# Optimization experiments

Hardware: AMD Instinct MI355X
Metric: run time of the kernel (lower is better)

## Reference

```python
import jax, jax.numpy as jnp
import numpy as np

PERIOD = 15          # hardcoded in the torch module's forward: STL(series, 15)
N_SEASONAL = 7       # statsmodels STL default seasonal smoother length
N_TREND = 29         # smallest odd >= 1.5*p/(1-1.5/7) = 28.64 -> 29 (statsmodels default)
N_LOWPASS = 17       # smallest odd > period (statsmodels default)
N_INNER = 2          # statsmodels: robust=False -> 2 inner iterations, 0 outer


def _loess_matrix(n, q, ts):
    """Dense linear operator for degree-1 LOESS smoothing of a length-n series
    evaluated at (possibly out-of-range) integer positions ts. Non-robust LOESS is
    linear in y, so smoothing == matmul with this constant matrix."""
    M = np.zeros((len(ts), n), dtype=np.float64)
    qq = min(q, n)
    for i, t in enumerate(ts):
        left = int(np.clip(t - (q - 1) // 2, 0, n - qq))
        right = left + qq - 1
        h = max(t - left, right - t)
        if q > n:
            h += (q - n) / 2.0
        xs = np.arange(left, right + 1, dtype=np.float64)
        w = np.clip(1.0 - (np.abs(xs - t) / h) ** 3, 0.0, None) ** 3  # tricube
        w = w / w.sum()
        xbar = (w * xs).sum()
        var = (w * (xs - xbar) ** 2).sum()
        a = w.copy()
        if var > 1e-12:  # degree-1 local linear fit; fall back to deg-0 if degenerate
            a = w * (1.0 + (t - xbar) * (xs - xbar) / var)
        M[i, left:right + 1] = a
    return M.astype(np.float32)


def _ma(x, k):
    """Moving average of window k along last axis (valid mode)."""
    cs = jnp.cumsum(x, axis=-1)
    cs = jnp.concatenate([jnp.zeros(x.shape[:-1] + (1,), x.dtype), cs], axis=-1)
    return (cs[..., k:] - cs[..., :-k]) / k


def setup_inputs() -> dict:
    key = jax.random.key(0)
    x = jax.random.normal(key, (128, 480, 256), dtype=jnp.float32)  # [B, T, C]
    return {"x": x}


def reference(x):
    B, T, Cc = x.shape
    p = PERIOD
    n_sub = T // p  # cycle-subseries length; T chosen divisible by period

    # Constant LOESS smoothing operators (numpy, baked in as jit constants)
    M_seas = jnp.asarray(_loess_matrix(n_sub, N_SEASONAL, np.arange(-1, n_sub + 1)))  # (n_sub+2, n_sub)
    M_lp = jnp.asarray(_loess_matrix(T, N_LOWPASS, np.arange(T)))                     # (T, T)
    M_trend = jnp.asarray(_loess_matrix(T, N_TREND, np.arange(T)))                    # (T, T)

    y = jnp.transpose(x, (0, 2, 1))  # [B, C, T]
    trend = jnp.zeros_like(y)
    seasonal = jnp.zeros_like(y)

    for _ in range(N_INNER):  # STL inner loop (Cleveland 1990, non-robust)
        # 1. detrend
        D = y - trend
        # 2. cycle-subseries LOESS smoothing, extended one period each side
        Dsub = D.reshape(B, Cc, n_sub, p)                      # subseries along axis 2
        Cext = jnp.einsum('sn,bcnp->bcsp', M_seas, Dsub)       # [B,C,n_sub+2,p]
        Cext = Cext.reshape(B, Cc, (n_sub + 2) * p)            # time order, length T+2p
        # 3. low-pass: MA(p) x2, MA(3), then LOESS(n_l)
        lp = _ma(_ma(_ma(Cext, p), p), 3)                      # length T
        L = jnp.einsum('tn,bcn->bct', M_lp, lp)
        # 4. seasonal = smoothed subseries (center T) minus low-pass
        seasonal = Cext[..., p:p + T] - L
        # 5+6. deseasonalize and trend LOESS
        trend = jnp.einsum('tn,bcn->bct', M_trend, y - seasonal)

    resid = y - seasonal - trend
    seas_plus_resid = jnp.transpose(seasonal + resid, (0, 2, 1))  # [B, T, C]
    trend_out = jnp.transpose(trend, (0, 2, 1))
    return (seas_plus_resid, trend_out)
```

## Files before the change

### kernel.cpp

```cpp
#include <hip/hip_runtime.h>
#include <hip/hip_bf16.h>
#include <stdint.h>

#define TLEN 480
#define NB 128
#define NC 256

typedef short bf16x8 __attribute__((ext_vector_type(8)));
typedef float f32x4 __attribute__((ext_vector_type(4)));

__device__ inline unsigned short f2bf(float f) {
    union { float f; uint32_t u; } v; v.f = f;
    uint32_t u = v.u;
    return (unsigned short)((u + 0x7fffu + ((u >> 16) & 1u)) >> 16);
}

__device__ void loess_row(int t, int n, int q, float* row) {
    int qq = q < n ? q : n;
    int left = t - (q - 1) / 2;
    if (left < 0) left = 0;
    if (left > n - qq) left = n - qq;
    int right = left + qq - 1;
    int h = (t - left) > (right - t) ? (t - left) : (right - t);
    double w[29];
    double wsum = 0.0;
    for (int i = 0; i < qq; ++i) {
        double dist = fabs((double)(left + i - t)) / (double)h;
        double u = 1.0 - dist * dist * dist;
        if (u < 0.0) u = 0.0;
        double wv = u * u * u;
        w[i] = wv; wsum += wv;
    }
    for (int i = 0; i < qq; ++i) w[i] /= wsum;
    double xbar = 0.0;
    for (int i = 0; i < qq; ++i) xbar += w[i] * (double)(left + i);
    double var = 0.0;
    for (int i = 0; i < qq; ++i) { double d = (double)(left + i) - xbar; var += w[i] * d * d; }
    if (var > 1e-12) {
        double tb = (double)t - xbar;
        for (int i = 0; i < qq; ++i) {
            double d = (double)(left + i) - xbar;
            row[left + i] = (float)(w[i] * (1.0 + tb * d / var));
        }
    } else {
        for (int i = 0; i < qq; ++i) row[left + i] = (float)w[i];
    }
}

__global__ void k_zero(float* p, int n) {
    int id = blockIdx.x * 256 + threadIdx.x;
    if (id < n) p[id] = 0.0f;
}

__global__ void k_loess(float* Ms, float* w3, float* Mlp, float* Mt) {
    int i = threadIdx.x;
    if (i < 34) {
        loess_row(i - 1, 32, 7, Ms + i * 32);
    } else if (i < 34 + 480) {
        int t = i - 34;
        loess_row(t, TLEN, 17, Mlp + (size_t)t * TLEN);
    } else if (i < 34 + 960) {
        int t = i - 514;
        loess_row(t, TLEN, 29, Mt + (size_t)t * TLEN);
    } else if (i == 1000) {
        for (int d = 0; d <= 30; ++d) {
            int cnt = 0;
            for (int c = 0; c < 3; ++c)
                for (int a = 0; a < 15; ++a) {
                    int b = d - a - c;
                    if (b >= 0 && b < 15) cnt++;
                }
            w3[d] = (float)((double)cnt / 675.0);
        }
    }
}

__global__ void k_G(const float* __restrict__ Ms, const float* __restrict__ w3, float* __restrict__ G) {
    int id = blockIdx.x * 256 + threadIdx.x;
    if (id >= TLEN * TLEN) return;
    int i = id / TLEN, u = id - i * TLEN;
    int ju = u % 15, nu = u / 15;
    float acc = 0.0f;
    for (int s = 0; s < 34; ++s) {
        int d = s * 15 + ju - i;
        if (d >= 0 && d <= 30) acc += Ms[s * 32 + nu] * w3[d];
    }
    G[id] = acc;
}

__global__ void k_S(const float* __restrict__ Ms, const float* __restrict__ Mlp,
                    const float* __restrict__ G, float* __restrict__ S) {
    int id = blockIdx.x * 256 + threadIdx.x;
    if (id >= TLEN * TLEN) return;
    int t = id / TLEN, u = id - t * TLEN;
    int lo = t - 8;
    if (lo < 0) lo = 0;
    if (lo > TLEN - 17) lo = TLEN - 17;
    float acc = 0.0f;
    for (int k = 0; k < 17; ++k)
        acc += Mlp[(size_t)t * TLEN + lo + k] * G[(size_t)(lo + k) * TLEN + u];
    float val = -acc;
    if (t % 15 == u % 15) val += Ms[(1 + t / 15) * 32 + (u / 15)];
    S[id] = val;
}

__global__ void k_VU(const float* __restrict__ Mt, const float* __restrict__ S,
                     float* __restrict__ U, float* __restrict__ V) {
    int id = blockIdx.x * 256 + threadIdx.x;
    if (id >= TLEN * TLEN) return;
    int t = id / TLEN, u = id - t * TLEN;
    int lo = t - 14;
    if (lo < 0) lo = 0;
    if (lo > TLEN - 29) lo = TLEN - 29;
    float acc = 0.0f;
    for (int k = 0; k < 29; ++k)
        acc += Mt[(size_t)t * TLEN + lo + k] * S[(size_t)(lo + k) * TLEN + u];
    V[id] = acc;
    U[id] = Mt[id] - acc;
}

__global__ void k_A(const float* __restrict__ U, const float* __restrict__ V,
                    unsigned short* __restrict__ Abf) {
    __shared__ float Vs[16][17];
    __shared__ float Us[16][17];
    int tx = threadIdx.x, ty = threadIdx.y;
    int u = blockIdx.x * 16 + tx;
    int t = blockIdx.y * 16 + ty;
    float acc = 0.0f;
    for (int kt = 0; kt < 30; ++kt) {
        Vs[ty][tx] = V[(size_t)t * TLEN + kt * 16 + tx];
        Us[ty][tx] = U[(size_t)(kt * 16 + ty) * TLEN + u];
        __syncthreads();
        #pragma unroll
        for (int e = 0; e < 16; ++e) acc += Vs[ty][e] * Us[e][tx];
        __syncthreads();
    }
    Abf[(size_t)t * TLEN + u] = f2bf(U[(size_t)t * TLEN + u] + acc);
}

__global__ void k_tr(const float* __restrict__ x, unsigned short* __restrict__ Xt) {
    __shared__ unsigned short Tt[32 * 36];
    int b = blockIdx.z, s0 = blockIdx.y * 32, c0 = blockIdx.x * 32;
    int i = threadIdx.x;
    int r = i >> 3, cg = i & 7;
    float4 v = *(const float4*)(x + (((size_t)b * TLEN + s0 + r) * NC + c0 + cg * 4));
    Tt[(cg * 4 + 0) * 36 + r] = f2bf(v.x);
    Tt[(cg * 4 + 1) * 36 + r] = f2bf(v.y);
    Tt[(cg * 4 + 2) * 36 + r] = f2bf(v.z);
    Tt[(cg * 4 + 3) * 36 + r] = f2bf(v.w);
    __syncthreads();
    int cl = i >> 3, ch = i & 7;
    ushort4 o = *(const ushort4*)&Tt[cl * 36 + ch * 4];
    *(ushort4*)(Xt + (((size_t)b * NC + c0 + cl) * TLEN + s0 + ch * 4)) = o;
}

__global__ __launch_bounds__(256, 2)
void k_gemm(const unsigned short* __restrict__ A, const unsigned short* __restrict__ Xt,
            const float* __restrict__ x, float* __restrict__ out0, float* __restrict__ out1) {
    int b = blockIdx.y;
    int t0 = blockIdx.x * 48;
    int tid = threadIdx.x;
    int wave = tid >> 6, lane = tid & 63;
    int lane15 = lane & 15, quad = lane >> 4;
    int cbase = wave * 64;

    const unsigned short* ap[3];
    #pragma unroll
    for (int i = 0; i < 3; ++i)
        ap[i] = A + (size_t)(t0 + i * 16 + lane15) * TLEN + quad * 8;
    const unsigned short* bp[4];
    #pragma unroll
    for (int j = 0; j < 4; ++j)
        bp[j] = Xt + ((size_t)b * NC + cbase + j * 16 + lane15) * TLEN + quad * 8;

    f32x4 acc[3][4] = {};
    for (int k0 = 0; k0 < TLEN; k0 += 32) {
        bf16x8 af[3], bf[4];
        #pragma unroll
        for (int i = 0; i < 3; ++i) af[i] = *(const bf16x8*)(ap[i] + k0);
        #pragma unroll
        for (int j = 0; j < 4; ++j) bf[j] = *(const bf16x8*)(bp[j] + k0);
        #pragma unroll
        for (int i = 0; i < 3; ++i)
            #pragma unroll
            for (int j = 0; j < 4; ++j)
                acc[i][j] = __builtin_amdgcn_mfma_f32_16x16x32_bf16(af[i], bf[j], acc[i][j], 0, 0, 0);
    }

    #pragma unroll
    for (int i = 0; i < 3; ++i) {
        #pragma unroll
        for (int r = 0; r < 4; ++r) {
            int t = t0 + i * 16 + quad * 4 + r;
            size_t rowbase = ((size_t)b * TLEN + t) * NC;
            #pragma unroll
            for (int j = 0; j < 4; ++j) {
                int c = cbase + j * 16 + lane15;
                float v = acc[i][j][r];
                out1[rowbase + c] = v;
                out0[rowbase + c] = x[rowbase + c] - v;
            }
        }
    }
}

extern "C" void kernel_launch(void* const* d_in, const int* in_sizes, int n_in,
                              void* d_out, int out_size, void* d_ws, size_t ws_size,
                              hipStream_t stream) {
    const float* x = (const float*)d_in[0];
    float* out0 = (float*)d_out;
    float* out1 = (float*)d_out + (size_t)NB * TLEN * NC;

    char* ws = (char*)d_ws;
    size_t oXt = 0;
    size_t oMs = 31457280;
    size_t oW3 = oMs + 4352;
    size_t oLp = oW3 + 128;
    size_t oMt = oLp + 921600;
    size_t oG  = oMt + 921600;
    size_t oS  = oG + 921600;
    size_t oU  = oS + 921600;
    size_t oV  = oU + 921600;
    size_t oA  = oV + 921600;

    unsigned short* Xt = (unsigned short*)(ws + oXt);
    float* Ms  = (float*)(ws + oMs);
    float* w3  = (float*)(ws + oW3);
    float* Mlp = (float*)(ws + oLp);
    float* Mt  = (float*)(ws + oMt);
    float* G   = (float*)(ws + oG);
    float* S   = (float*)(ws + oS);
    float* U   = (float*)(ws + oU);
    float* V   = (float*)(ws + oV);
    unsigned short* Abf = (unsigned short*)(ws + oA);

    int nzero = (4352 + 128 + 921600 * 2) / 4;
    k_zero<<<(nzero + 255) / 256, 256, 0, stream>>>((float*)(ws + oMs), nzero);
    k_loess<<<1, 1024, 0, stream>>>(Ms, w3, Mlp, Mt);
    k_G<<<900, 256, 0, stream>>>(Ms, w3, G);
    k_S<<<900, 256, 0, stream>>>(Ms, Mlp, G, S);
    k_VU<<<900, 256, 0, stream>>>(Mt, S, U, V);
    k_A<<<dim3(30, 30), dim3(16, 16), 0, stream>>>(U, V, Abf);
    k_tr<<<dim3(8, 15, NB), 256, 0, stream>>>(x, Xt);
    k_gemm<<<dim3(10, NB), 256, 0, stream>>>(Abf, Xt, x, out0, out1);
}
```

Baseline: 316.4 us.

## Compact LOESS weights, fuse G into S, swap GEMM operands for vector stores

Stores the LOESS operators as compact banded weights instead of dense 480x480 matrices. This drops the zeroing kernel and the separate G kernel by computing the G entries inline in k_S. The GEMM swaps operand roles so each lane's accumulator holds four consecutive channels, which allows float4 loads of x and float4 stores of both outputs instead of scalar ones. It also changes the grid order to batch-major and raises launch bounds to 4 blocks per unit, which risks register pressure.

New measurement: 289.5 us. -8.5%, faster.

```diff
diff --git a/kernel.cpp b/kernel.cpp
--- a/kernel.cpp
+++ b/kernel.cpp
@@ -8,61 +8,66 @@
 
 typedef short bf16x8 __attribute__((ext_vector_type(8)));
 typedef float f32x4 __attribute__((ext_vector_type(4)));
-
-__device__ inline unsigned short f2bf(float f) {
+typedef unsigned short u16;
+
+__device__ inline u16 f2bf(float f) {
     union { float f; uint32_t u; } v; v.f = f;
     uint32_t u = v.u;
-    return (unsigned short)((u + 0x7fffu + ((u >> 16) & 1u)) >> 16);
-}
-
-__device__ void loess_row(int t, int n, int q, float* row) {
-    int qq = q < n ? q : n;
+    return (u16)((u + 0x7fffu + ((u >> 16) & 1u)) >> 16);
+}
+
+__device__ int loess_w(int t, int n, int q, float* out) {
     int left = t - (q - 1) / 2;
     if (left < 0) left = 0;
-    if (left > n - qq) left = n - qq;
-    int right = left + qq - 1;
+    if (left > n - q) left = n - q;
+    int right = left + q - 1;
     int h = (t - left) > (right - t) ? (t - left) : (right - t);
     double w[29];
     double wsum = 0.0;
-    for (int i = 0; i < qq; ++i) {
+    for (int i = 0; i < q; ++i) {
         double dist = fabs((double)(left + i - t)) / (double)h;
         double u = 1.0 - dist * dist * dist;
         if (u < 0.0) u = 0.0;
         double wv = u * u * u;
         w[i] = wv; wsum += wv;
     }
-    for (int i = 0; i < qq; ++i) w[i] /= wsum;
+    for (int i = 0; i < q; ++i) w[i] /= wsum;
     double xbar = 0.0;
-    for (int i = 0; i < qq; ++i) xbar += w[i] * (double)(left + i);
+    for (int i = 0; i < q; ++i) xbar += w[i] * (double)(left + i);
     double var = 0.0;
-    for (int i = 0; i < qq; ++i) { double d = (double)(left + i) - xbar; var += w[i] * d * d; }
+    for (int i = 0; i < q; ++i) { double d = (double)(left + i) - xbar; var += w[i] * d * d; }
     if (var > 1e-12) {
         double tb = (double)t - xbar;
-        for (int i = 0; i < qq; ++i) {
+        for (int i = 0; i < q; ++i) {
             double d = (double)(left + i) - xbar;
-            row[left + i] = (float)(w[i] * (1.0 + tb * d / var));
+            out[i] = (float)(w[i] * (1.0 + tb * d / var));
         }
     } else {
-        for (int i = 0; i < qq; ++i) row[left + i] = (float)w[i];
-    }
-}
-
-__global__ void k_zero(float* p, int n) {
-    int id = blockIdx.x * 256 + threadIdx.x;
-    if (id < n) p[id] = 0.0f;
-}
-
-__global__ void k_loess(float* Ms, float* w3, float* Mlp, float* Mt) {
-    int i = threadIdx.x;
-    if (i < 34) {
-        loess_row(i - 1, 32, 7, Ms + i * 32);
-    } else if (i < 34 + 480) {
-        int t = i - 34;
-        loess_row(t, TLEN, 17, Mlp + (size_t)t * TLEN);
-    } else if (i < 34 + 960) {
-        int t = i - 514;
-        loess_row(t, TLEN, 29, Mt + (size_t)t * TLEN);
-    } else if (i == 1000) {
+        for (int i = 0; i < q; ++i) out[i] = (float)w[i];
+    }
+    return left;
+}
+
+__global__ void k_loess(float* Ms, float* w3, float* MlpC, float* MtC) {
+    int gid = blockIdx.x * 256 + threadIdx.x;
+    if (gid < 34) {
+        float wl[7];
+        int left = loess_w(gid - 1, 32, 7, wl);
+        float* row = Ms + gid * 32;
+        #pragma unroll
+        for (int i = 0; i < 32; ++i) row[i] = 0.0f;
+        for (int i = 0; i < 7; ++i) row[left + i] = wl[i];
+    } else if (gid < 514) {
+        int t = gid - 34;
+        float wl[17];
+        loess_w(t, TLEN, 17, wl);
+        for (int i = 0; i < 17; ++i) MlpC[t * 17 + i] = wl[i];
+    } else if (gid < 994) {
+        int t = gid - 514;
+        float wl[29];
+        loess_w(t, TLEN, 29, wl);
+        for (int i = 0; i < 29; ++i) MtC[t * 29 + i] = wl[i];
+    } else if (gid == 994) {
         for (int d = 0; d <= 30; ++d) {
             int cnt = 0;
             for (int c = 0; c < 3; ++c)
@@ -75,52 +80,52 @@
     }
 }
 
-__global__ void k_G(const float* __restrict__ Ms, const float* __restrict__ w3, float* __restrict__ G) {
-    int id = blockIdx.x * 256 + threadIdx.x;
-    if (id >= TLEN * TLEN) return;
-    int i = id / TLEN, u = id - i * TLEN;
-    int ju = u % 15, nu = u / 15;
-    float acc = 0.0f;
-    for (int s = 0; s < 34; ++s) {
-        int d = s * 15 + ju - i;
-        if (d >= 0 && d <= 30) acc += Ms[s * 32 + nu] * w3[d];
-    }
-    G[id] = acc;
-}
-
-__global__ void k_S(const float* __restrict__ Ms, const float* __restrict__ Mlp,
-                    const float* __restrict__ G, float* __restrict__ S) {
+__global__ void k_S(const float* __restrict__ Ms, const float* __restrict__ w3,
+                    const float* __restrict__ MlpC, float* __restrict__ S) {
     int id = blockIdx.x * 256 + threadIdx.x;
     if (id >= TLEN * TLEN) return;
     int t = id / TLEN, u = id - t * TLEN;
-    int lo = t - 8;
-    if (lo < 0) lo = 0;
-    if (lo > TLEN - 17) lo = TLEN - 17;
+    int nu = u / 15, ju = u - nu * 15;
+    int slp = t - 8;
+    if (slp < 0) slp = 0;
+    if (slp > TLEN - 17) slp = TLEN - 17;
     float acc = 0.0f;
-    for (int k = 0; k < 17; ++k)
-        acc += Mlp[(size_t)t * TLEN + lo + k] * G[(size_t)(lo + k) * TLEN + u];
+    for (int k = 0; k < 17; ++k) {
+        int i = slp + k;
+        int s_lo = (i - ju + 14) / 15;
+        float g = 0.0f;
+        #pragma unroll
+        for (int ds = 0; ds < 3; ++ds) {
+            int s = s_lo + ds;
+            int d = s * 15 + ju - i;
+            if (s >= 0 && s < 34 && d >= 0 && d <= 30)
+                g += Ms[s * 32 + nu] * w3[d];
+        }
+        acc += MlpC[t * 17 + k] * g;
+    }
     float val = -acc;
-    if (t % 15 == u % 15) val += Ms[(1 + t / 15) * 32 + (u / 15)];
+    if (t % 15 == ju) val += Ms[(1 + t / 15) * 32 + nu];
     S[id] = val;
 }
 
-__global__ void k_VU(const float* __restrict__ Mt, const float* __restrict__ S,
+__global__ void k_VU(const float* __restrict__ MtC, const float* __restrict__ S,
                      float* __restrict__ U, float* __restrict__ V) {
     int id = blockIdx.x * 256 + threadIdx.x;
     if (id >= TLEN * TLEN) return;
     int t = id / TLEN, u = id - t * TLEN;
-    int lo = t - 14;
-    if (lo < 0) lo = 0;
-    if (lo > TLEN - 29) lo = TLEN - 29;
+    int st = t - 14;
+    if (st < 0) st = 0;
+    if (st > TLEN - 29) st = TLEN - 29;
     float acc = 0.0f;
     for (int k = 0; k < 29; ++k)
-        acc += Mt[(size_t)t * TLEN + lo + k] * S[(size_t)(lo + k) * TLEN + u];
+        acc += MtC[t * 29 + k] * S[(size_t)(st + k) * TLEN + u];
+    float mt = (u >= st && u < st + 29) ? MtC[t * 29 + (u - st)] : 0.0f;
     V[id] = acc;
-    U[id] = Mt[id] - acc;
+    U[id] = mt - acc;
 }
 
 __global__ void k_A(const float* __restrict__ U, const float* __restrict__ V,
-                    unsigned short* __restrict__ Abf) {
+                    u16* __restrict__ Abf) {
     __shared__ float Vs[16][17];
     __shared__ float Us[16][17];
     int tx = threadIdx.x, ty = threadIdx.y;
@@ -138,8 +143,8 @@
     Abf[(size_t)t * TLEN + u] = f2bf(U[(size_t)t * TLEN + u] + acc);
 }
 
-__global__ void k_tr(const float* __restrict__ x, unsigned short* __restrict__ Xt) {
-    __shared__ unsigned short Tt[32 * 36];
+__global__ void k_tr(const float* __restrict__ x, u16* __restrict__ Xt) {
+    __shared__ u16 Tt[32 * 36];
     int b = blockIdx.z, s0 = blockIdx.y * 32, c0 = blockIdx.x * 32;
     int i = threadIdx.x;
     int r = i >> 3, cg = i & 7;
@@ -154,52 +159,50 @@
     *(ushort4*)(Xt + (((size_t)b * NC + c0 + cl) * TLEN + s0 + ch * 4)) = o;
 }
 
-__global__ __launch_bounds__(256, 2)
-void k_gemm(const unsigned short* __restrict__ A, const unsigned short* __restrict__ Xt,
+__global__ __launch_bounds__(256, 4)
+void k_gemm(const u16* __restrict__ A, const u16* __restrict__ Xt,
             const float* __restrict__ x, float* __restrict__ out0, float* __restrict__ out1) {
-    int b = blockIdx.y;
-    int t0 = blockIdx.x * 48;
+    int b = blockIdx.x;
+    int t0 = blockIdx.y * 48;
     int tid = threadIdx.x;
     int wave = tid >> 6, lane = tid & 63;
     int lane15 = lane & 15, quad = lane >> 4;
-    int cbase = wave * 64;
-
-    const unsigned short* ap[3];
+    int cw = wave * 64;
+
+    const u16* ap[4];
     #pragma unroll
-    for (int i = 0; i < 3; ++i)
-        ap[i] = A + (size_t)(t0 + i * 16 + lane15) * TLEN + quad * 8;
-    const unsigned short* bp[4];
+    for (int i = 0; i < 4; ++i)
+        ap[i] = Xt + ((size_t)b * NC + cw + i * 16 + lane15) * TLEN + quad * 8;
+    const u16* bp[3];
     #pragma unroll
-    for (int j = 0; j < 4; ++j)
-        bp[j] = Xt + ((size_t)b * NC + cbase + j * 16 + lane15) * TLEN + quad * 8;
-
-    f32x4 acc[3][4] = {};
+    for (int j = 0; j < 3; ++j)
+        bp[j] = A + (size_t)(t0 + j * 16 + lane15) * TLEN + quad * 8;
+
+    f32x4 acc[4][3] = {};
     for (int k0 = 0; k0 < TLEN; k0 += 32) {
-        bf16x8 af[3], bf[4];
-        #pragma unroll
-        for (int i = 0; i < 3; ++i) af[i] = *(const bf16x8*)(ap[i] + k0);
-        #pragma unroll
-        for (int j = 0; j < 4; ++j) bf[j] = *(const bf16x8*)(bp[j] + k0);
-        #pragma unroll
-        for (int i = 0; i < 3; ++i)
+        bf16x8 af[4], bfr[3];
+        #pragma unroll
+        for (int i = 0; i < 4; ++i) af[i] = *(const bf16x8*)(ap[i] + k0);
+        #pragma unroll
+        for (int j = 0; j < 3; ++j) bfr[j] = *(const bf16x8*)(bp[j] + k0);
+        #pragma unroll
+        for (int i = 0; i < 4; ++i)
             #pragma unroll
-            for (int j = 0; j < 4; ++j)
-                acc[i][j] = __builtin_amdgcn_mfma_f32_16x16x32_bf16(af[i], bf[j], acc[i][j], 0, 0, 0);
+            for (int j = 0; j < 3; ++j)
+                acc[i][j] = __builtin_amdgcn_mfma_f32_16x16x32_bf16(af[i], bfr[j], acc[i][j], 0, 0, 0);
     }
 
     #pragma unroll
-    for (int i = 0; i < 3; ++i) {
-        #pragma unroll
-        for (int r = 0; r < 4; ++r) {
-            int t = t0 + i * 16 + quad * 4 + r;
-            size_t rowbase = ((size_t)b * TLEN + t) * NC;
-            #pragma unroll
-            for (int j = 0; j < 4; ++j) {
-                int c = cbase + j * 16 + lane15;
-                float v = acc[i][j][r];
-                out1[rowbase + c] = v;
-                out0[rowbase + c] = x[rowbase + c] - v;
-            }
+    for (int i = 0; i < 4; ++i) {
+        #pragma unroll
+        for (int j = 0; j < 3; ++j) {
+            int t = t0 + j * 16 + lane15;
+            int c = cw + i * 16 + quad * 4;
+            size_t base = ((size_t)b * TLEN + t) * NC + c;
+            float4 xv = *(const float4*)(x + base);
+            float4 tv = make_float4(acc[i][j][0], acc[i][j][1], acc[i][j][2], acc[i][j][3]);
+            *(float4*)(out1 + base) = tv;
+            *(float4*)(out0 + base) = make_float4(xv.x - tv.x, xv.y - tv.y, xv.z - tv.z, xv.w - tv.w);
         }
     }
 }
@@ -212,35 +215,30 @@
     float* out1 = (float*)d_out + (size_t)NB * TLEN * NC;
 
     char* ws = (char*)d_ws;
-    size_t oXt = 0;
-    size_t oMs = 31457280;
-    size_t oW3 = oMs + 4352;
-    size_t oLp = oW3 + 128;
-    size_t oMt = oLp + 921600;
-    size_t oG  = oMt + 921600;
-    size_t oS  = oG + 921600;
-    size_t oU  = oS + 921600;
-    size_t oV  = oU + 921600;
-    size_t oA  = oV + 921600;
-
-    unsigned short* Xt = (unsigned short*)(ws + oXt);
-    float* Ms  = (float*)(ws + oMs);
-    float* w3  = (float*)(ws + oW3);
-    float* Mlp = (float*)(ws + oLp);
-    float* Mt  = (float*)(ws + oMt);
-    float* G   = (float*)(ws + oG);
-    float* S   = (float*)(ws + oS);
-    float* U   = (float*)(ws + oU);
-    float* V   = (float*)(ws + oV);
-    unsigned short* Abf = (unsigned short*)(ws + oA);
-
-    int nzero = (4352 + 128 + 921600 * 2) / 4;
-    k_zero<<<(nzero + 255) / 256, 256, 0, stream>>>((float*)(ws + oMs), nzero);
-    k_loess<<<1, 1024, 0, stream>>>(Ms, w3, Mlp, Mt);
-    k_G<<<900, 256, 0, stream>>>(Ms, w3, G);
-    k_S<<<900, 256, 0, stream>>>(Ms, Mlp, G, S);
-    k_VU<<<900, 256, 0, stream>>>(Mt, S, U, V);
+    size_t oXt  = 0;
+    size_t oMs  = 31457280;
+    size_t oW3  = oMs + 4352;
+    size_t oLpC = oW3 + 128;
+    size_t oMtC = oLpC + 32640;
+    size_t oS   = oMtC + 55680;
+    size_t oU   = oS + 921600;
+    size_t oV   = oU + 921600;
+    size_t oA   = oV + 921600;
+
+    u16*   Xt   = (u16*)(ws + oXt);
+    float* Ms   = (float*)(ws + oMs);
+    float* w3   = (float*)(ws + oW3);
+    float* MlpC = (float*)(ws + oLpC);
+    float* MtC  = (float*)(ws + oMtC);
+    float* S    = (float*)(ws + oS);
+    float* U    = (float*)(ws + oU);
+    float* V    = (float*)(ws + oV);
+    u16*   Abf  = (u16*)(ws + oA);
+
+    k_loess<<<4, 256, 0, stream>>>(Ms, w3, MlpC, MtC);
+    k_S<<<900, 256, 0, stream>>>(Ms, w3, MlpC, S);
+    k_VU<<<900, 256, 0, stream>>>(MtC, S, U, V);
     k_A<<<dim3(30, 30), dim3(16, 16), 0, stream>>>(U, V, Abf);
     k_tr<<<dim3(8, 15, NB), 256, 0, stream>>>(x, Xt);
-    k_gemm<<<dim3(10, NB), 256, 0, stream>>>(Abf, Xt, x, out0, out1);
-}
+    k_gemm<<<dim3(NB, 10), 256, 0, stream>>>(Abf, Xt, x, out0, out1);
+}
```
